# Kernel optimization log

Measured on AMD Instinct MI355X. Metric: run time of the kernel, lower is better.

The kernel has to match this reference:

```python
import jax, jax.numpy as jnp
import numpy as np

DIST_THRESH = 2.5


def _level_losses(lvl_cls, lvl_reg, gt_boxes, gt_labels):
    # lvl_cls: [B, HW, nc], lvl_reg: [B, HW, 4], gt_boxes: [B, N, 4], gt_labels: [B, N]
    gt_xy = gt_boxes[..., :2]            # [B, N, 2]
    pred_xy = lvl_reg[..., :2]           # [B, HW, 2]
    # squared euclidean distances [B, N, HW] (cdist equivalent; min/argmin unaffected by sqrt)
    d2 = jnp.sum((gt_xy[:, :, None, :] - pred_xy[:, None, :, :]) ** 2, axis=-1)
    min_d2 = jnp.min(d2, axis=2)         # [B, N]
    matches = jnp.argmin(d2, axis=2)     # [B, N]
    valid = jnp.sqrt(min_d2) < DIST_THRESH  # [B, N] bool
    # gather matched predictions per gt
    g_cls = jnp.take_along_axis(lvl_cls, matches[..., None], axis=1)   # [B, N, nc]
    g_reg = jnp.take_along_axis(lvl_reg, matches[..., None], axis=1)   # [B, N, 4]
    # cross entropy (reduction='none'), summed over valid matches
    logp = jax.nn.log_softmax(g_cls, axis=-1)
    ce = -jnp.take_along_axis(logp, gt_labels[..., None], axis=-1)[..., 0]  # [B, N]
    l1 = jnp.abs(g_reg - gt_boxes).sum(axis=-1)                             # [B, N]
    w = valid.astype(lvl_cls.dtype)
    return (ce * w).sum(), (l1 * w).sum(), w.sum()


def setup_inputs() -> dict:
    key = jax.random.key(0)
    ks = jax.random.split(key, 8)
    B, N, nc = 16, 128, 80
    hws = [25600, 6400, 1600]
    inp = {}
    for i, hw in enumerate(hws):
        inp[f"pred_cls_{i}"] = jax.random.normal(ks[i], (B, hw, nc), dtype=jnp.float32)
        inp[f"pred_reg_{i}"] = jax.random.normal(ks[3 + i], (B, hw, 4), dtype=jnp.float32)
    inp["gt_boxes"] = jax.random.normal(ks[6], (B, N, 4), dtype=jnp.float32)
    inp["gt_labels"] = jax.random.randint(ks[7], (B, N), 0, nc)
    return inp


def reference(pred_cls_0, pred_cls_1, pred_cls_2,
              pred_reg_0, pred_reg_1, pred_reg_2,
              gt_boxes, gt_labels):
    cls_list = [pred_cls_0, pred_cls_1, pred_cls_2]
    reg_list = [pred_reg_0, pred_reg_1, pred_reg_2]
    cls_loss = jnp.zeros((), jnp.float32)
    reg_loss = jnp.zeros((), jnp.float32)
    num_pos = jnp.zeros((), jnp.float32)
    for lvl_cls, lvl_reg in zip(cls_list, reg_list):
        c, r, n = _level_losses(lvl_cls, lvl_reg, gt_boxes, gt_labels)
        cls_loss = cls_loss + c
        reg_loss = reg_loss + r
        num_pos = num_pos + n
    denom = jnp.maximum(num_pos, 1.0)
    return cls_loss / denom, reg_loss / denom, num_pos
```

## Files before the change

### kernel.cpp

```cpp
#include <hip/hip_runtime.h>
#include <cstdint>
#include <cstddef>

#define NTH 256
#define NGT 128
#define BATCH 16
#define NC 80
#define G 16
#define NCHUNK (NGT / G)
#define HW0 25600
#define HW1 6400
#define HW2 1600
#define NBLK (3 * BATCH * NCHUNK)

__device__ __forceinline__ unsigned long long umin64(unsigned long long a, unsigned long long b) {
    return a < b ? a : b;
}

#define EVAL(px, py, idx_) do {                                                   \
    _Pragma("unroll")                                                             \
    for (int g = 0; g < G; ++g) {                                                 \
        float dx = gx[g] - (px), dy = gy[g] - (py);                               \
        float d2 = dx * dx + dy * dy;                                             \
        unsigned long long key =                                                  \
            ((unsigned long long)__float_as_uint(d2) << 32) | (unsigned)(idx_);   \
        kmin[g] = umin64(kmin[g], key);                                           \
    } } while (0)

__global__ __launch_bounds__(NTH) void scan_loss_kernel(
    const float* __restrict__ cls0, const float* __restrict__ cls1, const float* __restrict__ cls2,
    const float* __restrict__ reg0, const float* __restrict__ reg1, const float* __restrict__ reg2,
    const float* __restrict__ gt_boxes, const int* __restrict__ gt_labels,
    float* __restrict__ partl)
{
    const int x = blockIdx.x;
    const int lvl = x >> 7;
    const int y = x & 127;
    const int b = y >> 3, chunk = y & 7;

    const float* cls; const float* reg; int HW;
    if (lvl == 0)      { cls = cls0; reg = reg0; HW = HW0; }
    else if (lvl == 1) { cls = cls1; reg = reg1; HW = HW1; }
    else               { cls = cls2; reg = reg2; HW = HW2; }

    const int tid = threadIdx.x, wave = tid >> 6, lane = tid & 63;
    const int n0 = chunk * G;

    float gx[G], gy[G];
#pragma unroll
    for (int g = 0; g < G; ++g) {
        const float* gb = gt_boxes + (size_t)(b * NGT + n0 + g) * 4;
        gx[g] = gb[0]; gy[g] = gb[1];
    }

    unsigned long long kmin[G];
#pragma unroll
    for (int g = 0; g < G; ++g) kmin[g] = ~0ull;

    const float4* base = reinterpret_cast<const float4*>(reg) + (size_t)b * HW;
    for (int i = tid; i < HW; i += NTH) {
        float4 p = base[i];
        EVAL(p.x, p.y, i);
    }

#pragma unroll
    for (int g = 0; g < G; ++g) {
#pragma unroll
        for (int off = 32; off >= 1; off >>= 1) {
            unsigned long long o = __shfl_down(kmin[g], off, 64);
            kmin[g] = umin64(kmin[g], o);
        }
    }

    __shared__ unsigned long long smem[G][4];
    if (lane == 0) {
#pragma unroll
        for (int g = 0; g < G; ++g) smem[g][wave] = kmin[g];
    }
    __syncthreads();

    __shared__ unsigned long long keyf[G];
    if (tid < G) {
        keyf[tid] = umin64(umin64(smem[tid][0], smem[tid][1]),
                           umin64(smem[tid][2], smem[tid][3]));
    }
    __syncthreads();

    float ce_acc = 0.0f, l1_acc = 0.0f, w_acc = 0.0f;
#pragma unroll
    for (int j = 0; j < 4; ++j) {
        const int g = wave * 4 + j;
        unsigned long long key = keyf[g];
        int match = (int)(unsigned)(key & 0xffffffffu);
        float d2min = __uint_as_float((unsigned)(key >> 32));
        bool valid = d2min < 6.25f;
        if (!valid) continue;

        const int n = n0 + g;
        const int label = gt_labels[b * NGT + n];
        const float* c = cls + ((size_t)b * HW + match) * NC;

        float x1 = c[lane];
        float x2 = (lane < NC - 64) ? c[64 + lane] : -INFINITY;
        float mx = fmaxf(x1, x2);
#pragma unroll
        for (int off = 32; off >= 1; off >>= 1) mx = fmaxf(mx, __shfl_xor(mx, off, 64));
        float s = expf(x1 - mx) + ((lane < NC - 64) ? expf(x2 - mx) : 0.0f);
#pragma unroll
        for (int off = 32; off >= 1; off >>= 1) s += __shfl_xor(s, off, 64);

        if (lane == 0) {
            ce_acc += -(c[label] - mx - logf(s));
            const float* gb = gt_boxes + (size_t)(b * NGT + n) * 4;
            const float* gr = reg + ((size_t)b * HW + match) * 4;
            l1_acc += fabsf(gr[0] - gb[0]) + fabsf(gr[1] - gb[1]) +
                      fabsf(gr[2] - gb[2]) + fabsf(gr[3] - gb[3]);
            w_acc += 1.0f;
        }
    }

    __shared__ float cw[4][3];
    if (lane == 0) { cw[wave][0] = ce_acc; cw[wave][1] = l1_acc; cw[wave][2] = w_acc; }
    __syncthreads();

    if (tid == 0) {
        float* o = partl + (size_t)blockIdx.x * 3;
        o[0] = cw[0][0] + cw[1][0] + cw[2][0] + cw[3][0];
        o[1] = cw[0][1] + cw[1][1] + cw[2][1] + cw[3][1];
        o[2] = cw[0][2] + cw[1][2] + cw[2][2] + cw[3][2];
    }
}

__global__ __launch_bounds__(NTH) void finalize_kernel(
    const float* __restrict__ partl, float* __restrict__ out)
{
    const int tid = threadIdx.x, wave = tid >> 6, lane = tid & 63;
    float ce = 0.0f, l1 = 0.0f, w = 0.0f;
    for (int i = tid; i < NBLK; i += NTH) {
        ce += partl[(size_t)i * 3 + 0];
        l1 += partl[(size_t)i * 3 + 1];
        w  += partl[(size_t)i * 3 + 2];
    }
#pragma unroll
    for (int off = 32; off >= 1; off >>= 1) {
        ce += __shfl_xor(ce, off, 64);
        l1 += __shfl_xor(l1, off, 64);
        w  += __shfl_xor(w,  off, 64);
    }
    __shared__ float sm[3][4];
    if (lane == 0) { sm[0][wave] = ce; sm[1][wave] = l1; sm[2][wave] = w; }
    __syncthreads();
    if (tid == 0) {
        float tce = sm[0][0] + sm[0][1] + sm[0][2] + sm[0][3];
        float tl1 = sm[1][0] + sm[1][1] + sm[1][2] + sm[1][3];
        float tw  = sm[2][0] + sm[2][1] + sm[2][2] + sm[2][3];
        float denom = fmaxf(tw, 1.0f);
        out[0] = tce / denom;
        out[1] = tl1 / denom;
        out[2] = tw;
    }
}

extern "C" void kernel_launch(void* const* d_in, const int* in_sizes, int n_in,
                              void* d_out, int out_size, void* d_ws, size_t ws_size,
                              hipStream_t stream) {
    const float* cls0 = nullptr; const float* cls1 = nullptr; const float* cls2 = nullptr;
    const float* reg0 = nullptr; const float* reg1 = nullptr; const float* reg2 = nullptr;
    const float* gt_boxes = nullptr; const int* gt_labels = nullptr;
    for (int i = 0; i < n_in; ++i) {
        switch (in_sizes[i]) {
            case BATCH * HW0 * NC: cls0 = (const float*)d_in[i]; break;
            case BATCH * HW1 * NC: cls1 = (const float*)d_in[i]; break;
            case BATCH * HW2 * NC: cls2 = (const float*)d_in[i]; break;
            case BATCH * HW0 * 4:  reg0 = (const float*)d_in[i]; break;
            case BATCH * HW1 * 4:  reg1 = (const float*)d_in[i]; break;
            case BATCH * HW2 * 4:  reg2 = (const float*)d_in[i]; break;
            case BATCH * NGT * 4:  gt_boxes = (const float*)d_in[i]; break;
            case BATCH * NGT:      gt_labels = (const int*)d_in[i]; break;
            default: break;
        }
    }

    float* partl = (float*)d_ws;

    scan_loss_kernel<<<NBLK, NTH, 0, stream>>>(
        cls0, cls1, cls2, reg0, reg1, reg2, gt_boxes, gt_labels, partl);

    finalize_kernel<<<1, NTH, 0, stream>>>(partl, (float*)d_out);
}
```

Baseline: 267.3 us.

## Split large-level scans across slices and fuse finalize via last-block atomics

Level 0 and level 1 scans are split into 8 and 2 HW slices, so more blocks share the work and the long level-0 blocks no longer set the kernel's critical path. Each slice writes its per-gt min key to workspace, and the last slice to finish, found with an atomic counter, merges the keys and computes the losses. The separate finalize kernel is folded in through a global done counter, and a memset resets the counters each call. This adds atomics, fences and a memset launch in exchange for better load balance and one fewer kernel launch.

Measured after the change: 307.0 us. 1.15x slower.

```diff
diff --git a/kernel.cpp b/kernel.cpp
--- a/kernel.cpp
+++ b/kernel.cpp
@@ -8,10 +8,24 @@
 #define NC 80
 #define G 16
 #define NCHUNK (NGT / G)
+#define NCHUNKS_TOTAL (3 * BATCH * NCHUNK)
 #define HW0 25600
 #define HW1 6400
 #define HW2 1600
-#define NBLK (3 * BATCH * NCHUNK)
+#define SL0 8
+#define SL1 2
+#define SL2 1
+#define MAXSL 8
+#define NB0 (BATCH * NCHUNK * SL0)
+#define NB1 (BATCH * NCHUNK * SL1)
+#define NB2 (BATCH * NCHUNK * SL2)
+#define GRID (NB0 + NB1 + NB2)
+
+#define CNT_OFF    0
+#define CNT_BYTES  ((NCHUNKS_TOTAL + 1) * (int)sizeof(unsigned int))
+#define PART_OFF   4096
+#define PART_BYTES (3 * BATCH * NGT * MAXSL * 8)
+#define PARTL_OFF  (PART_OFF + PART_BYTES)
 
 __device__ __forceinline__ unsigned long long umin64(unsigned long long a, unsigned long long b) {
     return a < b ? a : b;
@@ -27,24 +41,43 @@
         kmin[g] = umin64(kmin[g], key);                                           \
     } } while (0)
 
-__global__ __launch_bounds__(NTH) void scan_loss_kernel(
+__global__ __launch_bounds__(NTH) void mega_kernel(
     const float* __restrict__ cls0, const float* __restrict__ cls1, const float* __restrict__ cls2,
     const float* __restrict__ reg0, const float* __restrict__ reg1, const float* __restrict__ reg2,
     const float* __restrict__ gt_boxes, const int* __restrict__ gt_labels,
-    float* __restrict__ partl)
+    unsigned int* __restrict__ cnt,
+    unsigned int* __restrict__ done,
+    unsigned long long* __restrict__ part,
+    float* __restrict__ partl,
+    float* __restrict__ out)
 {
-    const int x = blockIdx.x;
-    const int lvl = x >> 7;
-    const int y = x & 127;
-    const int b = y >> 3, chunk = y & 7;
-
-    const float* cls; const float* reg; int HW;
-    if (lvl == 0)      { cls = cls0; reg = reg0; HW = HW0; }
-    else if (lvl == 1) { cls = cls1; reg = reg1; HW = HW1; }
-    else               { cls = cls2; reg = reg2; HW = HW2; }
-
+    int x = blockIdx.x;
+    int lvl, b, slice, chunk, HW, nsl;
+    const float4* src4;
+    const float* cls; const float* reg;
+    if (x < NB0) {
+        lvl = 0; b = x / (NCHUNK * SL0);
+        int r = x % (NCHUNK * SL0);
+        chunk = r % NCHUNK; slice = r / NCHUNK;
+        HW = HW0; nsl = SL0; reg = reg0; cls = cls0;
+    } else if (x < NB0 + NB1) {
+        int y = x - NB0;
+        lvl = 1; b = y / (NCHUNK * SL1);
+        int r = y % (NCHUNK * SL1);
+        chunk = r % NCHUNK; slice = r / NCHUNK;
+        HW = HW1; nsl = SL1; reg = reg1; cls = cls1;
+    } else {
+        int y = x - NB0 - NB1;
+        lvl = 2; b = y / NCHUNK; chunk = y % NCHUNK; slice = 0;
+        HW = HW2; nsl = SL2; reg = reg2; cls = cls2;
+    }
+    src4 = reinterpret_cast<const float4*>(reg);
+
+    const int seg = HW / nsl;
+    const int e0 = slice * seg, e1 = e0 + seg;
     const int tid = threadIdx.x, wave = tid >> 6, lane = tid & 63;
     const int n0 = chunk * G;
+    const int cg = (lvl * BATCH + b) * NCHUNK + chunk;
 
     float gx[G], gy[G];
 #pragma unroll
@@ -57,8 +90,8 @@
 #pragma unroll
     for (int g = 0; g < G; ++g) kmin[g] = ~0ull;
 
-    const float4* base = reinterpret_cast<const float4*>(reg) + (size_t)b * HW;
-    for (int i = tid; i < HW; i += NTH) {
+    const float4* base = src4 + (size_t)b * HW;
+    for (int i = e0 + tid; i < e1; i += NTH) {
         float4 p = base[i];
         EVAL(p.x, p.y, i);
     }
@@ -79,10 +112,30 @@
     }
     __syncthreads();
 
+    if (tid < G) {
+        unsigned long long key = umin64(umin64(smem[tid][0], smem[tid][1]),
+                                        umin64(smem[tid][2], smem[tid][3]));
+        part[((size_t)(lvl * BATCH + b) * NGT + n0 + tid) * MAXSL + slice] = key;
+    }
+    __syncthreads();
+
+    __shared__ int lastf;
+    if (tid == 0) {
+        __threadfence();
+        unsigned int old = atomicAdd(&cnt[cg], 1u);
+        lastf = (old == (unsigned)(nsl - 1));
+    }
+    __syncthreads();
+    if (!lastf) return;
+
+    __threadfence();
     __shared__ unsigned long long keyf[G];
     if (tid < G) {
-        keyf[tid] = umin64(umin64(smem[tid][0], smem[tid][1]),
-                           umin64(smem[tid][2], smem[tid][3]));
+        const unsigned long long* p =
+            part + ((size_t)(lvl * BATCH + b) * NGT + n0 + tid) * MAXSL;
+        unsigned long long k = p[0];
+        for (int s = 1; s < nsl; ++s) k = umin64(k, p[s]);
+        keyf[tid] = k;
     }
     __syncthreads();
 
@@ -93,8 +146,7 @@
         unsigned long long key = keyf[g];
         int match = (int)(unsigned)(key & 0xffffffffu);
         float d2min = __uint_as_float((unsigned)(key >> 32));
-        bool valid = d2min < 6.25f;
-        if (!valid) continue;
+        if (!(d2min < 6.25f)) continue;
 
         const int n = n0 + g;
         const int label = gt_labels[b * NGT + n];
@@ -123,20 +175,22 @@
     if (lane == 0) { cw[wave][0] = ce_acc; cw[wave][1] = l1_acc; cw[wave][2] = w_acc; }
     __syncthreads();
 
+    __shared__ int finalf;
     if (tid == 0) {
-        float* o = partl + (size_t)blockIdx.x * 3;
+        float* o = partl + (size_t)cg * 3;
         o[0] = cw[0][0] + cw[1][0] + cw[2][0] + cw[3][0];
         o[1] = cw[0][1] + cw[1][1] + cw[2][1] + cw[3][1];
         o[2] = cw[0][2] + cw[1][2] + cw[2][2] + cw[3][2];
-    }
-}
-
-__global__ __launch_bounds__(NTH) void finalize_kernel(
-    const float* __restrict__ partl, float* __restrict__ out)
-{
-    const int tid = threadIdx.x, wave = tid >> 6, lane = tid & 63;
+        __threadfence();
+        unsigned int old = atomicAdd(done, 1u);
+        finalf = (old == (unsigned)(NCHUNKS_TOTAL - 1));
+    }
+    __syncthreads();
+    if (!finalf) return;
+
+    __threadfence();
     float ce = 0.0f, l1 = 0.0f, w = 0.0f;
-    for (int i = tid; i < NBLK; i += NTH) {
+    for (int i = tid; i < NCHUNKS_TOTAL; i += NTH) {
         ce += partl[(size_t)i * 3 + 0];
         l1 += partl[(size_t)i * 3 + 1];
         w  += partl[(size_t)i * 3 + 2];
@@ -181,10 +235,15 @@
         }
     }
 
-    float* partl = (float*)d_ws;
-
-    scan_loss_kernel<<<NBLK, NTH, 0, stream>>>(
-        cls0, cls1, cls2, reg0, reg1, reg2, gt_boxes, gt_labels, partl);
-
-    finalize_kernel<<<1, NTH, 0, stream>>>(partl, (float*)d_out);
+    char* ws = (char*)d_ws;
+    unsigned int* cnt = (unsigned int*)(ws + CNT_OFF);
+    unsigned int* done = cnt + NCHUNKS_TOTAL;
+    unsigned long long* part = (unsigned long long*)(ws + PART_OFF);
+    float* partl = (float*)(ws + PARTL_OFF);
+
+    hipMemsetAsync(cnt, 0, CNT_BYTES, stream);
+
+    mega_kernel<<<GRID, NTH, 0, stream>>>(
+        cls0, cls1, cls2, reg0, reg1, reg2, gt_boxes, gt_labels,
+        cnt, done, part, partl, (float*)d_out);
 }
```
